# Optimization experiments

Hardware: AMD Instinct MI355X
Metric: run time of the kernel (lower is better)

The kernel has to match this reference:

```python
import jax, jax.numpy as jnp
import numpy as np

EPS = 1e-5
N_SEGMENT = 8


def _bn(x, g, b, m, v):
    # x: (nt, c) or (nt, c, h, w); params: (c,)
    shape = (1, -1) + (1,) * (x.ndim - 2)
    scale = (g * jax.lax.rsqrt(v + EPS)).reshape(shape)
    return (x - m.reshape(shape)) * scale + b.reshape(shape)


def setup_inputs() -> dict:
    key = jax.random.key(0)
    ks = jax.random.split(key, 20)
    c, c8 = 256, 32
    nt, h, w = 128, 28, 28
    inp = {
        'x': jax.random.normal(ks[0], (nt, c, h, w), jnp.float32),
        'wq': jax.random.normal(ks[1], (c8, c), jnp.float32) * 0.05,
        'bq': jax.random.normal(ks[2], (c8,), jnp.float32) * 0.05,
        'gq': jax.random.uniform(ks[3], (c8,), jnp.float32),
        'betaq': jax.random.normal(ks[4], (c8,), jnp.float32) * 0.05,
        'mq': jax.random.normal(ks[5], (c8,), jnp.float32) * 0.05,
        'vq': jax.random.uniform(ks[6], (c8,), jnp.float32),
        'wk': jax.random.normal(ks[7], (c8, c), jnp.float32) * 0.05,
        'bk': jax.random.normal(ks[8], (c8,), jnp.float32) * 0.05,
        'gk': jax.random.uniform(ks[9], (c8,), jnp.float32),
        'betak': jax.random.normal(ks[10], (c8,), jnp.float32) * 0.05,
        'mk': jax.random.normal(ks[11], (c8,), jnp.float32) * 0.05,
        'vk': jax.random.uniform(ks[12], (c8,), jnp.float32),
        'wi': jax.random.normal(ks[13], (c, c8), jnp.float32) * 0.05,
        'bi': jax.random.normal(ks[14], (c,), jnp.float32) * 0.05,
        'gi': jax.random.uniform(ks[15], (c,), jnp.float32),
        'betai': jax.random.normal(ks[16], (c,), jnp.float32) * 0.05,
        'mi': jax.random.normal(ks[17], (c,), jnp.float32) * 0.05,
        'vi': jax.random.uniform(ks[18], (c,), jnp.float32),
    }
    return inp


def reference(x, wq, bq, gq, betaq, mq, vq, wk, bk, gk, betak, mk, vk,
              wi, bi, gi, betai, mi, vi):
    nt, c, h, w = x.shape
    T = N_SEGMENT
    nb = nt // T
    # conv1x1 + BN(eval) + ReLU, then global avg pool -> (nt, c//n_div)
    q = jnp.einsum('nchw,oc->nohw', x, wq) + bq[None, :, None, None]
    q = jax.nn.relu(_bn(q, gq, betaq, mq, vq)).mean(axis=(2, 3))
    k = jnp.einsum('nchw,oc->nohw', x, wk) + bk[None, :, None, None]
    k = jax.nn.relu(_bn(k, gk, betak, mk, vk)).mean(axis=(2, 3))
    # Trans_att(out_q, out_q, out_v): q and k branches are BOTH q; v is k branch
    q3 = q.reshape(nb, T, -1)
    v3 = k.reshape(nb, T, -1)
    att = -jnp.einsum('bic,bjc->bij', q3, q3)  # (nb, T, T)
    att = jax.nn.softmax(att, axis=1)          # softmax over dim 1 as in torch
    q_upd = jnp.einsum('bij,bjc->bic', att, v3) + v3  # (nb, T, c8)
    q_upd = q_upd.reshape(nt, -1)
    # conv_inflate (1x1 conv on (nt, c8, 1, 1)) + BN + ReLU
    y = q_upd @ wi.T + bi
    y = jax.nn.relu(_bn(y, gi, betai, mi, vi))
    gate = jax.nn.sigmoid(y)                    # (nt, c)
    return gate[:, :, None, None] * x
```

## Files before the change

kernel.cpp:

```cpp
#include <hip/hip_runtime.h>
#include <cstdint>
#include <cstddef>

#define EPSV 1e-5f
typedef uint32_t u32;
typedef unsigned short u16;
typedef __attribute__((ext_vector_type(8))) short bf16x8;
typedef __attribute__((ext_vector_type(4))) float f32x4;

__device__ __forceinline__ u16 f2b(float x){ union { float f; u32 i; } v; v.f=x; u32 t=v.i; return (u16)((t + 0x7fffu + ((t>>16)&1u))>>16); }

__global__ __launch_bounds__(256) void k_prep(
    const float* __restrict__ wq, const float* __restrict__ bq, const float* __restrict__ gq,
    const float* __restrict__ betaq, const float* __restrict__ mq, const float* __restrict__ vq,
    const float* __restrict__ wk, const float* __restrict__ bk, const float* __restrict__ gk,
    const float* __restrict__ betak, const float* __restrict__ mk, const float* __restrict__ vk,
    u16* __restrict__ Wswz, float* __restrict__ D)
{
  const int idx = blockIdx.x*256 + threadIdx.x;
  const int j = idx & 7, lane = (idx >> 3) & 63, nt = (idx >> 9) & 3, kk = idx >> 11;
  const int c = kk*32 + ((lane >> 4) << 3) + j;
  const int o = nt*16 + (lane & 15);
  float w, g, v;
  if (o < 32) { w = wq[o*256 + c];      g = gq[o];    v = vq[o]; }
  else        { w = wk[(o-32)*256 + c]; g = gk[o-32]; v = vk[o-32]; }
  Wswz[idx] = f2b(w * (g * rsqrtf(v + EPSV)));
  if (idx < 64) {
    float gg,b,be,m,vv;
    if (idx < 32) { gg=gq[idx];    b=bq[idx];    be=betaq[idx];    m=mq[idx];    vv=vq[idx]; }
    else          { gg=gk[idx-32]; b=bk[idx-32]; be=betak[idx-32]; m=mk[idx-32]; vv=vk[idx-32]; }
    const float s = gg * rsqrtf(vv + EPSV);
    D[idx] = (b - m)*s + be;
  }
}

__global__ __launch_bounds__(256) void k_stageA(
    const float* __restrict__ x, const u16* __restrict__ Wswz, const float* __restrict__ D,
    float* __restrict__ qk_part)
{
  __shared__ float red[256];
  const int tid = threadIdx.x;
  const int n = blockIdx.x / 13, g = blockIdx.x % 13;
  const int wv = tid >> 6, lane = tid & 63;
  const int tile = g*4 + wv;
  const bool active = (tile < 49);

  float s4[4] = {0.f, 0.f, 0.f, 0.f};
  if (active) {
    const int px = tile*16 + (lane & 15);
    const float* xr = x + (size_t)n*200704 + px;
    const int krow = (lane >> 4) * 8;
    const bf16x8* Wf = (const bf16x8*)Wswz;

    f32x4 acc[4];
#pragma unroll
    for (int nt = 0; nt < 4; ++nt) acc[nt] = (f32x4){0.f, 0.f, 0.f, 0.f};

    float a[8], an[8];
#pragma unroll
    for (int j = 0; j < 8; ++j) a[j] = xr[(size_t)(krow + j)*784];

#pragma unroll
    for (int kk = 0; kk < 8; ++kk) {
      if (kk < 7) {
#pragma unroll
        for (int j = 0; j < 8; ++j) an[j] = xr[(size_t)((kk+1)*32 + krow + j)*784];
      }
      bf16x8 af;
#pragma unroll
      for (int j = 0; j < 8; ++j) af[j] = (short)f2b(a[j]);
#pragma unroll
      for (int nt = 0; nt < 4; ++nt) {
        const bf16x8 bf = Wf[(kk*4 + nt)*64 + lane];
        acc[nt] = __builtin_amdgcn_mfma_f32_16x16x32_bf16(af, bf, acc[nt], 0, 0, 0);
      }
#pragma unroll
      for (int j = 0; j < 8; ++j) a[j] = an[j];
    }

#pragma unroll
    for (int nt = 0; nt < 4; ++nt) {
      const float d = D[nt*16 + (lane & 15)];
      float s = 0.f;
#pragma unroll
      for (int r = 0; r < 4; ++r) s += fmaxf(acc[nt][r] + d, 0.f);
      s += __shfl_down(s, 16, 64);
      s += __shfl_down(s, 32, 64);
      s4[nt] = s;
    }
  }

  if (lane < 16) {
#pragma unroll
    for (int nt = 0; nt < 4; ++nt)
      red[wv*64 + nt*16 + lane] = active ? s4[nt] : 0.f;
  }
  __syncthreads();
  if (tid < 64) {
    qk_part[(size_t)(n*13 + g)*64 + tid] =
        red[tid] + red[64+tid] + red[128+tid] + red[192+tid];
  }
}

__global__ __launch_bounds__(256) void k_stageB(
    const float* __restrict__ qk_part,
    const float* __restrict__ wi, const float* __restrict__ bi, const float* __restrict__ gi,
    const float* __restrict__ betai, const float* __restrict__ mi, const float* __restrict__ vi,
    float* __restrict__ gate)
{
  __shared__ float ql[8][32], vl[8][32], attl[8][8], qul[8][32];
  const int tid = threadIdx.x;
  const int b = blockIdx.x;

  {
    const int i = tid >> 5, c = tid & 31;
    const int n = b*8 + i;
    float sq = 0.f, sv = 0.f;
#pragma unroll
    for (int qq = 0; qq < 13; ++qq) {
      sq += qk_part[(size_t)(n*13 + qq)*64 + c];
      sv += qk_part[(size_t)(n*13 + qq)*64 + 32 + c];
    }
    ql[i][c] = sq * (1.f/784.f);
    vl[i][c] = sv * (1.f/784.f);
  }
  __syncthreads();

  if (tid < 64) {
    const int i = tid >> 3, j = tid & 7;
    float d = 0.f;
#pragma unroll
    for (int c = 0; c < 32; ++c) d += ql[i][c]*ql[j][c];
    float a = -d;
    float m = a;
    m = fmaxf(m, __shfl_xor(m, 8, 64));
    m = fmaxf(m, __shfl_xor(m, 16, 64));
    m = fmaxf(m, __shfl_xor(m, 32, 64));
    const float e = __expf(a - m);
    float s = e;
    s += __shfl_xor(s, 8, 64);
    s += __shfl_xor(s, 16, 64);
    s += __shfl_xor(s, 32, 64);
    attl[i][j] = e / s;
  }
  __syncthreads();

  {
    const int i = tid >> 5, c = tid & 31;
    float acc = vl[i][c];
#pragma unroll
    for (int j = 0; j < 8; ++j) acc = fmaf(attl[i][j], vl[j][c], acc);
    qul[i][c] = acc;
  }
  __syncthreads();

  {
    const int cout = tid;
    float w[32];
#pragma unroll
    for (int k = 0; k < 32; ++k) w[k] = wi[cout*32 + k];
    const float s  = gi[cout] * rsqrtf(vi[cout] + EPSV);
    const float dd = (bi[cout] - mi[cout]) * s + betai[cout];
#pragma unroll
    for (int i = 0; i < 8; ++i) {
      float y = 0.f;
#pragma unroll
      for (int k = 0; k < 32; ++k) y = fmaf(qul[i][k], w[k], y);
      const float t = fmaxf(fmaf(y, s, dd), 0.f);
      gate[(size_t)(b*8 + i)*256 + cout] = 1.f / (1.f + __expf(-t));
    }
  }
}

__global__ __launch_bounds__(256) void k_gateMul(
    const float* __restrict__ x, const float* __restrict__ gate, float* __restrict__ out)
{
  const u32 nchunk = 128u*256u*196u;
  const u32 stride = gridDim.x * 256u;
  for (u32 q = blockIdx.x*256u + threadIdx.x; q < nchunk; q += stride) {
    const u32 cn = q / 196u;
    const float g = gate[cn];
    const float4 v = reinterpret_cast<const float4*>(x)[q];
    float4 o4;
    o4.x = v.x * g; o4.y = v.y * g; o4.z = v.z * g; o4.w = v.w * g;
    reinterpret_cast<float4*>(out)[q] = o4;
  }
}

extern "C" void kernel_launch(void* const* d_in, const int* in_sizes, int n_in,
                              void* d_out, int out_size, void* d_ws, size_t ws_size,
                              hipStream_t stream) {
  const float* x    = (const float*)d_in[0];
  const float* wq   = (const float*)d_in[1];
  const float* bq   = (const float*)d_in[2];
  const float* gq   = (const float*)d_in[3];
  const float* betaq= (const float*)d_in[4];
  const float* mq   = (const float*)d_in[5];
  const float* vq   = (const float*)d_in[6];
  const float* wk   = (const float*)d_in[7];
  const float* bk   = (const float*)d_in[8];
  const float* gk   = (const float*)d_in[9];
  const float* betak= (const float*)d_in[10];
  const float* mk   = (const float*)d_in[11];
  const float* vk   = (const float*)d_in[12];
  const float* wi   = (const float*)d_in[13];
  const float* bi   = (const float*)d_in[14];
  const float* gi   = (const float*)d_in[15];
  const float* betai= (const float*)d_in[16];
  const float* mi   = (const float*)d_in[17];
  const float* vi   = (const float*)d_in[18];

  char* ws = (char*)d_ws;
  float* qk_part = (float*)(ws);
  float* gate    = (float*)(ws + 425984);
  u16*   Wswz    = (u16*)  (ws + 557056);
  float* Dc      = (float*)(ws + 589824);

  k_prep<<<64, 256, 0, stream>>>(wq,bq,gq,betaq,mq,vq, wk,bk,gk,betak,mk,vk, Wswz, Dc);
  k_stageA<<<1664, 256, 0, stream>>>(x, Wswz, Dc, qk_part);
  k_stageB<<<16, 256, 0, stream>>>(qk_part, wi,bi,gi,betai,mi,vi, gate);
  k_gateMul<<<2048, 256, 0, stream>>>(x, gate, (float*)d_out);
}
```

Measured before the change: 66.94 us.

## Fuse attention/gate computation into gate-multiply kernel, dropping stageB launch

Merges the small attention and inflate-conv kernel into the gate-multiply kernel. Each of the 2048 blocks recomputes the 8x8 attention for its batch group, then computes 16 gate values for its channel slice before scaling x. This removes one kernel launch and the gate round trip through global memory. In exchange the attention work is repeated in every block, and a serial prologue now sits ahead of the bandwidth-bound multiply.

```diff
diff --git a/kernel.cpp b/kernel.cpp
--- a/kernel.cpp
+++ b/kernel.cpp
@@ -102,24 +102,27 @@
   }
 }
 
-__global__ __launch_bounds__(256) void k_stageB(
-    const float* __restrict__ qk_part,
+__global__ __launch_bounds__(256) void k_gateMulB(
+    const float* __restrict__ x, const float* __restrict__ qk_part,
     const float* __restrict__ wi, const float* __restrict__ bi, const float* __restrict__ gi,
     const float* __restrict__ betai, const float* __restrict__ mi, const float* __restrict__ vi,
-    float* __restrict__ gate)
+    float* __restrict__ out)
 {
-  __shared__ float ql[8][32], vl[8][32], attl[8][8], qul[8][32];
+  __shared__ float ql[8][32], vl[8][32], attl[8][8], gl[16];
   const int tid = threadIdx.x;
-  const int b = blockIdx.x;
+  const int blk = blockIdx.x;
+  const int n  = blk >> 4;
+  const int c0 = (blk & 15) << 4;
+  const int b  = n >> 3, i0 = n & 7;
 
   {
     const int i = tid >> 5, c = tid & 31;
-    const int n = b*8 + i;
+    const int nn = b*8 + i;
     float sq = 0.f, sv = 0.f;
 #pragma unroll
     for (int qq = 0; qq < 13; ++qq) {
-      sq += qk_part[(size_t)(n*13 + qq)*64 + c];
-      sv += qk_part[(size_t)(n*13 + qq)*64 + 32 + c];
+      sq += qk_part[(size_t)(nn*13 + qq)*64 + c];
+      sv += qk_part[(size_t)(nn*13 + qq)*64 + 32 + c];
     }
     ql[i][c] = sq * (1.f/784.f);
     vl[i][c] = sv * (1.f/784.f);
@@ -145,45 +148,33 @@
   }
   __syncthreads();
 
-  {
-    const int i = tid >> 5, c = tid & 31;
-    float acc = vl[i][c];
-#pragma unroll
-    for (int j = 0; j < 8; ++j) acc = fmaf(attl[i][j], vl[j][c], acc);
-    qul[i][c] = acc;
-  }
-  __syncthreads();
-
-  {
-    const int cout = tid;
-    float w[32];
-#pragma unroll
-    for (int k = 0; k < 32; ++k) w[k] = wi[cout*32 + k];
+  if (tid < 16) {
+    const int cout = c0 + tid;
     const float s  = gi[cout] * rsqrtf(vi[cout] + EPSV);
     const float dd = (bi[cout] - mi[cout]) * s + betai[cout];
-#pragma unroll
-    for (int i = 0; i < 8; ++i) {
-      float y = 0.f;
-#pragma unroll
-      for (int k = 0; k < 32; ++k) y = fmaf(qul[i][k], w[k], y);
-      const float t = fmaxf(fmaf(y, s, dd), 0.f);
-      gate[(size_t)(b*8 + i)*256 + cout] = 1.f / (1.f + __expf(-t));
-    }
-  }
-}
-
-__global__ __launch_bounds__(256) void k_gateMul(
-    const float* __restrict__ x, const float* __restrict__ gate, float* __restrict__ out)
-{
-  const u32 nchunk = 128u*256u*196u;
-  const u32 stride = gridDim.x * 256u;
-  for (u32 q = blockIdx.x*256u + threadIdx.x; q < nchunk; q += stride) {
-    const u32 cn = q / 196u;
-    const float g = gate[cn];
-    const float4 v = reinterpret_cast<const float4*>(x)[q];
+    float y = 0.f;
+#pragma unroll
+    for (int k = 0; k < 32; ++k) {
+      float qu = vl[i0][k];
+#pragma unroll
+      for (int j = 0; j < 8; ++j) qu = fmaf(attl[i0][j], vl[j][k], qu);
+      y = fmaf(qu, wi[cout*32 + k], y);
+    }
+    const float t = fmaxf(fmaf(y, s, dd), 0.f);
+    gl[tid] = 1.f / (1.f + __expf(-t));
+  }
+  __syncthreads();
+
+  const float4* xb = reinterpret_cast<const float4*>(x)   + (size_t)(n*256 + c0)*196;
+  float4*       ob = reinterpret_cast<float4*>(out)       + (size_t)(n*256 + c0)*196;
+#pragma unroll 4
+  for (int q = tid; q < 3136; q += 256) {
+    const int row = q / 196;
+    const float g = gl[row];
+    const float4 v = xb[q];
     float4 o4;
     o4.x = v.x * g; o4.y = v.y * g; o4.z = v.z * g; o4.w = v.w * g;
-    reinterpret_cast<float4*>(out)[q] = o4;
+    ob[q] = o4;
   }
 }
 
@@ -212,12 +203,10 @@
 
   char* ws = (char*)d_ws;
   float* qk_part = (float*)(ws);
-  float* gate    = (float*)(ws + 425984);
-  u16*   Wswz    = (u16*)  (ws + 557056);
-  float* Dc      = (float*)(ws + 589824);
+  u16*   Wswz    = (u16*)  (ws + 425984);
+  float* Dc      = (float*)(ws + 458752);
 
   k_prep<<<64, 256, 0, stream>>>(wq,bq,gq,betaq,mq,vq, wk,bk,gk,betak,mk,vk, Wswz, Dc);
   k_stageA<<<1664, 256, 0, stream>>>(x, Wswz, Dc, qk_part);
-  k_stageB<<<16, 256, 0, stream>>>(qk_part, wi,bi,gi,betai,mi,vi, gate);
-  k_gateMul<<<2048, 256, 0, stream>>>(x, gate, (float*)d_out);
-}
+  k_gateMulB<<<2048, 256, 0, stream>>>(x, qk_part, wi,bi,gi,betai,mi,vi, (float*)d_out);
+}
```

New measurement: 65.62 us. 1.02x faster.
